# Kernel tuning notes

Measured on AMD Instinct MI355X. Metric: run time of the kernel, lower is better.

Reference implementation:

```python
import jax, jax.numpy as jnp
import numpy as np

BATCH = 2048
INPUT_DIM = 512
N = 8 ** 4  # reservoir_n ** reservoir_d = 4096
T = 16
NEG_SLOPE = 0.1
SPARSITY = 0.1  # fraction of nonzero entries in the pre-trained reservoir W


def setup_inputs() -> dict:
    key = jax.random.key(0)
    kx, kw, km = jax.random.split(key, 3)
    x = jax.random.normal(kx, (BATCH, INPUT_DIM), dtype=jnp.float32)
    # Sparse pre-trained reservoir weights; scale keeps spectral norm ~O(1)
    # so the T-step recurrence neither explodes nor vanishes.
    mask = (jax.random.uniform(km, (N, N)) < SPARSITY).astype(jnp.float32)
    W = jax.random.normal(kw, (N, N), dtype=jnp.float32) * mask / jnp.sqrt(SPARSITY * N)
    return {"x": x, "W": W}


def reference(x, W):
    # Pad input [B, input_dim] -> initial state S [B, N]
    S0 = jnp.pad(x, ((0, 0), (0, N - x.shape[1])))

    def step(S, _):
        S = jax.nn.leaky_relu(S @ W, negative_slope=NEG_SLOPE)
        return S, None

    S_final, _ = jax.lax.scan(step, S0, None, length=T)
    return S_final
```

## Files before the change

### kernel.cpp

```cpp
#include <hip/hip_runtime.h>


#define BATCH 2048
#define NDIM  4096
#define INDIM 512
#define BM 128
#define BN 128
#define BK 32

typedef _Float16 f16x8 __attribute__((ext_vector_type(8)));
typedef float    f32x4 __attribute__((ext_vector_type(4)));

__device__ __forceinline__ void async16(const void* gsrc, void* ldst) {
  const __attribute__((address_space(1))) unsigned int* g =
      (const __attribute__((address_space(1))) unsigned int*)gsrc;
  __attribute__((address_space(3))) unsigned int* l =
      (__attribute__((address_space(3))) unsigned int*)ldst;
  __builtin_amdgcn_global_load_lds(g, l, 16, 0, 0);
}

__device__ __forceinline__ f16x8 frag(const _Float16* s, int row, int q) {
  int ch = q ^ ((row >> 1) & 3);
  return *(const f16x8*)(s + row * BK + ch * 8);
}

__global__ void prep_x(const float* __restrict__ x,
                       _Float16* __restrict__ Sh, _Float16* __restrict__ Sl) {
  size_t i = (size_t)blockIdx.x * 256 + threadIdx.x;
  int b = (int)(i >> 12);
  int n = (int)(i & (NDIM - 1));
  float v = (n < INDIM) ? x[(size_t)b * INDIM + n] : 0.0f;
  _Float16 h = (_Float16)v;
  Sh[i] = h;
  Sl[i] = (_Float16)(v - (float)h);
}

__global__ void prep_w(const float* __restrict__ W,
                       _Float16* __restrict__ Wth, _Float16* __restrict__ Wtl) {
  __shared__ float tile[32][33];
  int k0 = blockIdx.y * 32, n0 = blockIdx.x * 32;
  int tx = threadIdx.x, ty = threadIdx.y;
  for (int r = 0; r < 4; r++) {
    int k = k0 + ty + r * 8;
    tile[ty + r * 8][tx] = W[(size_t)k * NDIM + n0 + tx];
  }
  __syncthreads();
  for (int r = 0; r < 4; r++) {
    int n = n0 + ty + r * 8;
    float v = tile[tx][ty + r * 8] * 256.0f;
    _Float16 h = (_Float16)v;
    Wth[(size_t)n * NDIM + k0 + tx] = h;
    Wtl[(size_t)n * NDIM + k0 + tx] = (_Float16)(v - (float)h);
  }
}

template <int MODE>
__global__ __launch_bounds__(256, 2) void step_kernel(
    const _Float16* __restrict__ Ah, const _Float16* __restrict__ Al,
    const _Float16* __restrict__ Bh, const _Float16* __restrict__ Bl,
    _Float16* __restrict__ Dh, _Float16* __restrict__ Dl,
    float* __restrict__ Dout, int k_len) {
  __shared__ _Float16 sAh[2][BM * BK];
  __shared__ _Float16 sAl[2][BM * BK];
  __shared__ _Float16 sBh[2][BN * BK];
  __shared__ _Float16 sBl[2][BN * BK];

  const int tid = threadIdx.x;
  const int lane = tid & 63;
  const int w = tid >> 6;
  const int wm = w >> 1;
  const int wn = w & 1;

  int id = blockIdx.x;
  int xcd = id & 7;
  int local = id >> 3;
  int lr = local & 7;
  int lc = local >> 3;
  int rb = (xcd & 1) * 8 + lr;
  int cb = (xcd >> 1) * 8 + lc;
  const int bm = rb * BM;
  const int bn = cb * BN;

  const int sr = lane >> 2;
  const int cl = lane & 3;
  const int fm = lane & 15;
  const int fq = lane >> 4;

  f32x4 acc[4][4];
  for (int i = 0; i < 4; i++)
    for (int j = 0; j < 4; j++) acc[i][j] = (f32x4){0.f, 0.f, 0.f, 0.f};

  auto stage = [&](int kt, int buf) {
    for (int q = 0; q < 2; q++) {
      int t = w * 2 + q;
      int r = t * 16 + sr;
      int cg = cl ^ ((r >> 1) & 3);
      size_t goA = (size_t)(bm + r) * NDIM + kt + cg * 8;
      size_t goB = (size_t)(bn + r) * NDIM + kt + cg * 8;
      int lo = r * BK + cl * 8;
      async16(Ah + goA, &sAh[buf][lo]);
      async16(Al + goA, &sAl[buf][lo]);
      async16(Bh + goB, &sBh[buf][lo]);
      async16(Bl + goB, &sBl[buf][lo]);
    }
  };

  stage(0, 0);
  asm volatile("s_waitcnt vmcnt(0)" ::: "memory");
  __syncthreads();

  const int nk = k_len / BK;
  for (int it = 0; it < nk; it++) {
    const int cur = it & 1;
    if (it + 1 < nk) stage((it + 1) * BK, cur ^ 1);

    f16x8 ah[4], al[4];
    for (int i = 0; i < 4; i++) {
      int r = wm * 64 + i * 16 + fm;
      ah[i] = frag(sAh[cur], r, fq);
      al[i] = frag(sAl[cur], r, fq);
    }
    for (int j = 0; j < 4; j++) {
      int r = wn * 64 + j * 16 + fm;
      f16x8 bh = frag(sBh[cur], r, fq);
      f16x8 bl = frag(sBl[cur], r, fq);
      for (int i = 0; i < 4; i++) {
        acc[i][j] = __builtin_amdgcn_mfma_f32_16x16x32_f16(ah[i], bh, acc[i][j], 0, 0, 0);
        acc[i][j] = __builtin_amdgcn_mfma_f32_16x16x32_f16(al[i], bh, acc[i][j], 0, 0, 0);
        acc[i][j] = __builtin_amdgcn_mfma_f32_16x16x32_f16(ah[i], bl, acc[i][j], 0, 0, 0);
      }
    }

    asm volatile("s_waitcnt vmcnt(0)" ::: "memory");
    __syncthreads();
  }

  const float inv = 1.0f / 256.0f;
  for (int i = 0; i < 4; i++) {
    for (int j = 0; j < 4; j++) {
      for (int e = 0; e < 4; e++) {
        int r = bm + wm * 64 + i * 16 + fq * 4 + e;
        int c = bn + wn * 64 + j * 16 + fm;
        float g = acc[i][j][e] * inv;
        float s = (g > 0.0f) ? g : 0.1f * g;
        if (MODE == 0) {
          _Float16 h = (_Float16)s;
          Dh[(size_t)r * NDIM + c] = h;
          Dl[(size_t)r * NDIM + c] = (_Float16)(s - (float)h);
        } else {
          Dout[(size_t)r * NDIM + c] = s;
        }
      }
    }
  }
}

extern "C" void kernel_launch(void* const* d_in, const int* in_sizes, int n_in,
                              void* d_out, int out_size, void* d_ws, size_t ws_size,
                              hipStream_t stream) {
  const float* x = (const float*)d_in[0];
  const float* W = (const float*)d_in[1];
  float* out = (float*)d_out;
  char* ws = (char*)d_ws;

  const size_t WT_BYTES = (size_t)NDIM * NDIM * 2;
  const size_t S_BYTES = (size_t)BATCH * NDIM * 2;
  _Float16* Wth = (_Float16*)ws;
  _Float16* Wtl = (_Float16*)(ws + WT_BYTES);
  _Float16* SAh = (_Float16*)(ws + 2 * WT_BYTES);
  _Float16* SAl = (_Float16*)(ws + 2 * WT_BYTES + S_BYTES);
  _Float16* SBh = (_Float16*)(ws + 2 * WT_BYTES + 2 * S_BYTES);
  _Float16* SBl = (_Float16*)(ws + 2 * WT_BYTES + 3 * S_BYTES);

  prep_x<<<(BATCH * NDIM) / 256, 256, 0, stream>>>(x, SAh, SAl);
  prep_w<<<dim3(NDIM / 32, NDIM / 32), dim3(32, 8), 0, stream>>>(W, Wth, Wtl);

  dim3 grid((NDIM / BN) * (BATCH / BM));
  for (int t = 1; t <= 16; t++) {
    const _Float16* ah = (t & 1) ? SAh : SBh;
    const _Float16* al = (t & 1) ? SAl : SBl;
    _Float16* dh = (t & 1) ? SBh : SAh;
    _Float16* dl = (t & 1) ? SBl : SAl;
    int klen = (t == 1) ? INDIM : NDIM;
    if (t < 16)
      step_kernel<0><<<grid, 256, 0, stream>>>(ah, al, Wth, Wtl, dh, dl, nullptr, klen);
    else
      step_kernel<1><<<grid, 256, 0, stream>>>(ah, al, Wth, Wtl, nullptr, nullptr, out, klen);
  }
}
```

Measured before the change: 2.683 ms.

## Double-buffer LDS fragments in registers to overlap LDS reads with MFMAs

The main loop is restructured into a two-stage register pipeline: fragments for the next K tile are read from LDS into a second register set while the MFMAs for the current tile run. Shared and global offsets are precomputed once per thread and the loops are fully unrolled. The explicit vmcnt waits before barriers are dropped, so correctness now depends on the barrier and fence waiting for the async global-to-LDS loads. Holding two full fragment sets in registers raises VGPR pressure.

```diff
diff --git a/kernel.cpp b/kernel.cpp
--- a/kernel.cpp
+++ b/kernel.cpp
@@ -17,11 +17,6 @@
   __attribute__((address_space(3))) unsigned int* l =
       (__attribute__((address_space(3))) unsigned int*)ldst;
   __builtin_amdgcn_global_load_lds(g, l, 16, 0, 0);
-}
-
-__device__ __forceinline__ f16x8 frag(const _Float16* s, int row, int q) {
-  int ch = q ^ ((row >> 1) & 3);
-  return *(const f16x8*)(s + row * BK + ch * 8);
 }
 
 __global__ void prep_x(const float* __restrict__ x,
@@ -53,6 +48,26 @@
     Wtl[(size_t)n * NDIM + k0 + tx] = (_Float16)(v - (float)h);
   }
 }
+
+#define READF(b, A, L, Bv, M)                          \
+  do {                                                 \
+    _Pragma("unroll") for (int i = 0; i < 4; i++) {    \
+      A[i]  = *(const f16x8*)&sAh[b][oA[i]];           \
+      L[i]  = *(const f16x8*)&sAl[b][oA[i]];           \
+      Bv[i] = *(const f16x8*)&sBh[b][oB[i]];           \
+      M[i]  = *(const f16x8*)&sBl[b][oB[i]];           \
+    }                                                  \
+  } while (0)
+
+#define MFMAS(A, L, Bv, M)                                                          \
+  do {                                                                              \
+    _Pragma("unroll") for (int j = 0; j < 4; j++)                                   \
+    _Pragma("unroll") for (int i = 0; i < 4; i++) {                                 \
+      acc[i][j] = __builtin_amdgcn_mfma_f32_16x16x32_f16(A[i], Bv[j], acc[i][j], 0, 0, 0); \
+      acc[i][j] = __builtin_amdgcn_mfma_f32_16x16x32_f16(L[i], Bv[j], acc[i][j], 0, 0, 0); \
+      acc[i][j] = __builtin_amdgcn_mfma_f32_16x16x32_f16(A[i], M[j], acc[i][j], 0, 0, 0); \
+    }                                                                               \
+  } while (0)
 
 template <int MODE>
 __global__ __launch_bounds__(256, 2) void step_kernel(
@@ -68,76 +83,87 @@
   const int tid = threadIdx.x;
   const int lane = tid & 63;
   const int w = tid >> 6;
-  const int wm = w >> 1;
-  const int wn = w & 1;
+  const int wm = w >> 1, wn = w & 1;
 
   int id = blockIdx.x;
-  int xcd = id & 7;
-  int local = id >> 3;
-  int lr = local & 7;
-  int lc = local >> 3;
-  int rb = (xcd & 1) * 8 + lr;
-  int cb = (xcd >> 1) * 8 + lc;
-  const int bm = rb * BM;
-  const int bn = cb * BN;
-
-  const int sr = lane >> 2;
-  const int cl = lane & 3;
-  const int fm = lane & 15;
-  const int fq = lane >> 4;
+  int xcd = id & 7, local = id >> 3;
+  int lr = local & 7, lc = local >> 3;
+  const int bm = ((xcd & 1) * 8 + lr) * BM;
+  const int bn = ((xcd >> 1) * 8 + lc) * BN;
+
+  const int sr = lane >> 2, cl = lane & 3;
+  const int fm = lane & 15, fq = lane >> 4;
+
+  int oA[4], oB[4];
+#pragma unroll
+  for (int i = 0; i < 4; i++) {
+    int rA = wm * 64 + i * 16 + fm;
+    oA[i] = rA * BK + (fq ^ ((rA >> 1) & 3)) * 8;
+    int rB = wn * 64 + i * 16 + fm;
+    oB[i] = rB * BK + (fq ^ ((rB >> 1) & 3)) * 8;
+  }
+
+  int r0 = w * 32 + sr, r1 = r0 + 16;
+  int cg0 = cl ^ ((r0 >> 1) & 3);
+  int cg1 = cl ^ ((r1 >> 1) & 3);
+  const size_t gA0 = (size_t)(bm + r0) * NDIM + cg0 * 8;
+  const size_t gA1 = (size_t)(bm + r1) * NDIM + cg1 * 8;
+  const size_t gB0 = (size_t)(bn + r0) * NDIM + cg0 * 8;
+  const size_t gB1 = (size_t)(bn + r1) * NDIM + cg1 * 8;
+  const int lo0 = r0 * BK + cl * 8;
+  const int lo1 = r1 * BK + cl * 8;
+
+  auto stage = [&](int kt, int b) {
+    async16(Ah + gA0 + kt, &sAh[b][lo0]);
+    async16(Ah + gA1 + kt, &sAh[b][lo1]);
+    async16(Al + gA0 + kt, &sAl[b][lo0]);
+    async16(Al + gA1 + kt, &sAl[b][lo1]);
+    async16(Bh + gB0 + kt, &sBh[b][lo0]);
+    async16(Bh + gB1 + kt, &sBh[b][lo1]);
+    async16(Bl + gB0 + kt, &sBl[b][lo0]);
+    async16(Bl + gB1 + kt, &sBl[b][lo1]);
+  };
 
   f32x4 acc[4][4];
+#pragma unroll
   for (int i = 0; i < 4; i++)
+#pragma unroll
     for (int j = 0; j < 4; j++) acc[i][j] = (f32x4){0.f, 0.f, 0.f, 0.f};
 
-  auto stage = [&](int kt, int buf) {
-    for (int q = 0; q < 2; q++) {
-      int t = w * 2 + q;
-      int r = t * 16 + sr;
-      int cg = cl ^ ((r >> 1) & 3);
-      size_t goA = (size_t)(bm + r) * NDIM + kt + cg * 8;
-      size_t goB = (size_t)(bn + r) * NDIM + kt + cg * 8;
-      int lo = r * BK + cl * 8;
-      async16(Ah + goA, &sAh[buf][lo]);
-      async16(Al + goA, &sAl[buf][lo]);
-      async16(Bh + goB, &sBh[buf][lo]);
-      async16(Bl + goB, &sBl[buf][lo]);
-    }
-  };
-
-  stage(0, 0);
-  asm volatile("s_waitcnt vmcnt(0)" ::: "memory");
+  f16x8 a0[4], l0[4], b0[4], m0[4];
+  f16x8 a1[4], l1[4], b1[4], m1[4];
+
+  const int nk = k_len / BK;
+
+  stage(0 * BK, 0);
+  stage(1 * BK, 1);
   __syncthreads();
-
-  const int nk = k_len / BK;
-  for (int it = 0; it < nk; it++) {
-    const int cur = it & 1;
-    if (it + 1 < nk) stage((it + 1) * BK, cur ^ 1);
-
-    f16x8 ah[4], al[4];
-    for (int i = 0; i < 4; i++) {
-      int r = wm * 64 + i * 16 + fm;
-      ah[i] = frag(sAh[cur], r, fq);
-      al[i] = frag(sAl[cur], r, fq);
-    }
+  READF(0, a0, l0, b0, m0);
+  __syncthreads();
+  stage(2 * BK, 0);
+
+  int it = 1;
+  for (; it + 1 < nk; it += 2) {
+    READF(1, a1, l1, b1, m1);
+    MFMAS(a0, l0, b0, m0);
+    __syncthreads();
+    if (it + 2 < nk) stage((it + 2) * BK, 1);
+
+    READF(0, a0, l0, b0, m0);
+    MFMAS(a1, l1, b1, m1);
+    __syncthreads();
+    if (it + 3 < nk) stage((it + 3) * BK, 0);
+  }
+  READF(1, a1, l1, b1, m1);
+  MFMAS(a0, l0, b0, m0);
+  MFMAS(a1, l1, b1, m1);
+
+  const float inv = 1.0f / 256.0f;
+#pragma unroll
+  for (int i = 0; i < 4; i++) {
+#pragma unroll
     for (int j = 0; j < 4; j++) {
-      int r = wn * 64 + j * 16 + fm;
-      f16x8 bh = frag(sBh[cur], r, fq);
-      f16x8 bl = frag(sBl[cur], r, fq);
-      for (int i = 0; i < 4; i++) {
-        acc[i][j] = __builtin_amdgcn_mfma_f32_16x16x32_f16(ah[i], bh, acc[i][j], 0, 0, 0);
-        acc[i][j] = __builtin_amdgcn_mfma_f32_16x16x32_f16(al[i], bh, acc[i][j], 0, 0, 0);
-        acc[i][j] = __builtin_amdgcn_mfma_f32_16x16x32_f16(ah[i], bl, acc[i][j], 0, 0, 0);
-      }
-    }
-
-    asm volatile("s_waitcnt vmcnt(0)" ::: "memory");
-    __syncthreads();
-  }
-
-  const float inv = 1.0f / 256.0f;
-  for (int i = 0; i < 4; i++) {
-    for (int j = 0; j < 4; j++) {
+#pragma unroll
       for (int e = 0; e < 4; e++) {
         int r = bm + wm * 64 + i * 16 + fq * 4 + e;
         int c = bn + wn * 64 + j * 16 + fm;
```

Result: faster. 2.415 ms (-10.0%).
